# Optimization experiments

Hardware: AMD Instinct MI355X
Metric: run time of the kernel (lower is better)

The kernel has to match this reference:

```python
import jax, jax.numpy as jnp
import numpy as np

NPROTOS = 40      # forced by init_offset_tensor reshape
NCLASS  = 512     # number of child classes
C       = 64      # genetic feature channels (pshape[0])
W       = 40      # genetic sequence width (hard-coded in offset tensor)
B       = 1024    # batch
P       = NPROTOS * NCLASS  # 20480 total prototypes
EPS     = 1e-12   # F.normalize eps


def _build_last_layer_weight():
    # match[j, j // nprotos] = 1, weight = match.T with zeros -> -0.5
    match = np.zeros((P, NCLASS), np.float32)
    match[np.arange(P), np.arange(P) // NPROTOS] = 1.0
    w = match.T.copy()
    w[w == 0] = -0.5
    return jnp.asarray(w)


def _build_offset_tensor():
    # arange2[i, j] = (i - j) % nprotos; nprotos == 40 so arange3 is empty
    i = np.arange(NPROTOS)[:, None]
    j = np.arange(NPROTOS)[None, :]
    ar2 = (i - j) % NPROTOS                                  # (40, 40)
    off = np.tile(ar2.reshape(NPROTOS, 1, 1, NPROTOS), (NCLASS, C, 1, 1))
    return jnp.asarray(off.astype(np.int32))                 # (P, C, 1, W)


def setup_inputs() -> dict:
    key = jax.random.key(0)
    k1, k2 = jax.random.split(key)
    conv_features = jax.random.normal(k1, (B, C, 1, W), dtype=jnp.float32)
    prototype = jax.random.uniform(k2, (P, C, 1, 1), dtype=jnp.float32)  # torch.rand
    return {
        "conv_features": conv_features,
        "prototype": prototype,
        "last_layer_weight": _build_last_layer_weight(),
        "offset_tensor": _build_offset_tensor(),
    }


def _l2norm(x, axis):
    # F.normalize: x / max(||x||_2, eps)
    return x / jnp.maximum(jnp.linalg.norm(x, axis=axis, keepdims=True), EPS)


def reference(conv_features, prototype, last_layer_weight, offset_tensor):
    sqrt_D = 1.0  # sqrt(pshape[1] * pshape[2]) = sqrt(1*1)
    x = _l2norm(conv_features, axis=1) / sqrt_D              # (B, C, 1, W)
    p = _l2norm(prototype, axis=1) / sqrt_D                  # (P, C, 1, 1)
    # pad prototypes to width W, then per-prototype spatial offset gather
    p = jnp.pad(p, ((0, 0), (0, 0), (0, 0), (0, W - 1)))     # (P, C, 1, W)
    p = jnp.take_along_axis(p, offset_tensor, axis=3)        # (P, C, 1, W)
    # conv2d with full-width kernel -> output (B, P, 1, 1); max_pool over 1x1 is identity
    sim = jnp.einsum('bchw,pchw->bp', x, p)                  # (B, P)
    min_distances = -sim                                     # view(-1, nclass*nprotos)
    logits = sim @ last_layer_weight.T                       # (B, NCLASS)
    return (logits, min_distances)
```

## Files before the change

### kernel.cpp

```cpp
#include <hip/hip_runtime.h>
#include <math.h>

#define NB 1024
#define NC 64
#define NW 40
#define NK 512
#define NP 20480
#define EPSF 1e-12f


__global__ __launch_bounds__(256) void knorm_p(const float* __restrict__ proto,
                                               float* __restrict__ pn) {
    int wave = threadIdx.x >> 6;
    int lane = threadIdx.x & 63;
    int p = blockIdx.x * 4 + wave;
    float v = proto[p * 64 + lane];
    float s = v * v;
#pragma unroll
    for (int off = 32; off >= 1; off >>= 1) s += __shfl_xor(s, off);
    float r = 1.0f / fmaxf(sqrtf(s), EPSF);
    int j = p % NW, k = p / NW;
    pn[(j * NK + k) * 64 + lane] = v * r;
}

__global__ __launch_bounds__(256) void knorm_x(const float* __restrict__ x,
                                               float* __restrict__ xn) {
    __shared__ float xs[64 * 41];
    __shared__ float rn[40];
    int b = blockIdx.x;
    const float* xb = x + b * (64 * 40);
    for (int t = threadIdx.x; t < 2560; t += 256) {
        int c = t / 40, w = t % 40;
        xs[c * 41 + w] = xb[t];
    }
    __syncthreads();
    if (threadIdx.x < 40) {
        int w = threadIdx.x;
        float s = 0.f;
#pragma unroll
        for (int c = 0; c < 64; ++c) { float v = xs[c * 41 + w]; s += v * v; }
        rn[w] = 1.0f / fmaxf(sqrtf(s), EPSF);
    }
    __syncthreads();
    for (int t = threadIdx.x; t < 2560; t += 256) {
        int w = t >> 6, c = t & 63;
        xn[(w * NB + b) * 64 + c] = xs[c * 41 + w] * rn[w];
    }
}

__global__ __launch_bounds__(256) void kgemm(const float* __restrict__ xn,
                                             const float* __restrict__ pn,
                                             float* __restrict__ simt) {
    __shared__ float4 Xs[128 * 16];
    __shared__ float4 Ps[128 * 16];
    int b0 = blockIdx.x * 128;
    int k0 = blockIdx.y * 128;
    int j  = blockIdx.z;
    const float4* xg = (const float4*)(xn + (size_t)(j * NB + b0) * 64);
    const float4* pg = (const float4*)(pn + (size_t)(j * NK + k0) * 64);
    for (int g = threadIdx.x; g < 2048; g += 256) {
        int row = g >> 4, c4 = g & 15;
        int idx = (row << 4) + (c4 ^ (row & 15));
        Xs[idx] = xg[g];
        Ps[idx] = pg[g];
    }
    __syncthreads();
    int tb = threadIdx.x >> 4, tk = threadIdx.x & 15;
    float acc[8][8];
#pragma unroll
    for (int i = 0; i < 8; ++i)
#pragma unroll
        for (int q = 0; q < 8; ++q) acc[i][q] = 0.f;

#pragma unroll 2
    for (int c4 = 0; c4 < 16; ++c4) {
        float4 xv[8], pv[8];
#pragma unroll
        for (int i = 0; i < 8; ++i) xv[i] = Xs[((tb + 16 * i) << 4) + (c4 ^ tb)];
#pragma unroll
        for (int q = 0; q < 8; ++q) pv[q] = Ps[((tk + 16 * q) << 4) + (c4 ^ tk)];
#pragma unroll
        for (int i = 0; i < 8; ++i)
#pragma unroll
            for (int q = 0; q < 8; ++q)
                acc[i][q] += xv[i].x * pv[q].x + xv[i].y * pv[q].y +
                             xv[i].z * pv[q].z + xv[i].w * pv[q].w;
    }

#pragma unroll
    for (int i = 0; i < 8; ++i) {
        int b = b0 + tb + 16 * i;
        float* dst = simt + (size_t)b * NP + j * NK + k0;
#pragma unroll
        for (int q = 0; q < 8; ++q) dst[tk + 16 * q] = acc[i][q];
    }
}

__global__ __launch_bounds__(1024) void ktrans(float* __restrict__ out) {
    __shared__ float row[512 * 41];
    __shared__ float red[1024];
    __shared__ float wsum[16];
    __shared__ float tshare;
    int b = blockIdx.x;
    float* md = out + 524288 + (size_t)b * NP;
    int k = threadIdx.x & 511;
    int jh = threadIdx.x >> 9;
    float racc = 0.f;
#pragma unroll 4
    for (int jj = 0; jj < 20; ++jj) {
        int j = jh * 20 + jj;
        float v = md[j * NK + k];
        row[k * 41 + j] = -v;
        racc += v;
    }
    red[threadIdx.x] = racc;
    float t = racc;
#pragma unroll
    for (int off = 32; off >= 1; off >>= 1) t += __shfl_xor(t, off);
    if ((threadIdx.x & 63) == 0) wsum[threadIdx.x >> 6] = t;
    __syncthreads();
    float rk = 0.f;
    if (threadIdx.x < 512) rk = red[threadIdx.x] + red[threadIdx.x + 512];
    if (threadIdx.x == 0) {
        float tt = 0.f;
#pragma unroll
        for (int i = 0; i < 16; ++i) tt += wsum[i];
        tshare = tt;
    }
    __syncthreads();
    if (threadIdx.x < 512)
        out[(size_t)b * NK + threadIdx.x] = 1.5f * rk - 0.5f * tshare;
    for (int t2 = threadIdx.x; t2 < NP; t2 += 1024) {
        int kk = t2 / 40, jj = t2 % 40;
        md[t2] = row[kk * 41 + jj];
    }
}

extern "C" void kernel_launch(void* const* d_in, const int* in_sizes, int n_in,
                              void* d_out, int out_size, void* d_ws, size_t ws_size,
                              hipStream_t stream) {
    (void)in_sizes; (void)n_in; (void)out_size; (void)ws_size;
    const float* conv  = (const float*)d_in[0];
    const float* proto = (const float*)d_in[1];
    float* out = (float*)d_out;
    float* ws = (float*)d_ws;
    float* pn = ws;
    float* xn = ws + 1310720;
    float* simt = out + 524288;

    knorm_p<<<5120, 256, 0, stream>>>(proto, pn);
    knorm_x<<<1024, 256, 0, stream>>>(conv, xn);
    kgemm<<<dim3(8, 4, 40), 256, 0, stream>>>(xn, pn, simt);
    ktrans<<<1024, 1024, 0, stream>>>(out);
}
```

Before: 370.5 us.

## Stage GEMM output in workspace and rework transpose kernel with float4 stores

The GEMM now writes its similarity tile to a separate workspace buffer with contiguous float4 stores, giving each thread eight adjacent prototype columns and a new LDS swizzle. The transpose/logit kernel reads from that buffer rather than transposing in place in the output. It drops from 1024 to 256 threads, processes 128 classes per pass through a small padded LDS tile, and writes the negated distances with float4 stores. This reduces LDS footprint and uncoalesced scalar traffic, at the cost of extra workspace and four barrier-separated passes per block.

```diff
diff --git a/kernel.cpp b/kernel.cpp
--- a/kernel.cpp
+++ b/kernel.cpp
@@ -60,7 +60,7 @@
     const float4* pg = (const float4*)(pn + (size_t)(j * NK + k0) * 64);
     for (int g = threadIdx.x; g < 2048; g += 256) {
         int row = g >> 4, c4 = g & 15;
-        int idx = (row << 4) + (c4 ^ (row & 15));
+        int idx = (row << 4) + (c4 ^ (row >> 3));
         Xs[idx] = xg[g];
         Ps[idx] = pg[g];
     }
@@ -72,67 +72,91 @@
 #pragma unroll
         for (int q = 0; q < 8; ++q) acc[i][q] = 0.f;
 
-#pragma unroll 2
     for (int c4 = 0; c4 < 16; ++c4) {
-        float4 xv[8], pv[8];
+        float4 xv[8];
 #pragma unroll
-        for (int i = 0; i < 8; ++i) xv[i] = Xs[((tb + 16 * i) << 4) + (c4 ^ tb)];
+        for (int i = 0; i < 8; ++i) {
+            int row = tb + 16 * i;
+            xv[i] = Xs[(row << 4) + (c4 ^ (row >> 3))];
+        }
 #pragma unroll
-        for (int q = 0; q < 8; ++q) pv[q] = Ps[((tk + 16 * q) << 4) + (c4 ^ tk)];
+        for (int q = 0; q < 8; ++q) {
+            int row = tk * 8 + q;
+            float4 pv = Ps[(row << 4) + (c4 ^ tk)];
 #pragma unroll
-        for (int i = 0; i < 8; ++i)
-#pragma unroll
-            for (int q = 0; q < 8; ++q)
-                acc[i][q] += xv[i].x * pv[q].x + xv[i].y * pv[q].y +
-                             xv[i].z * pv[q].z + xv[i].w * pv[q].w;
+            for (int i = 0; i < 8; ++i)
+                acc[i][q] += xv[i].x * pv.x + xv[i].y * pv.y +
+                             xv[i].z * pv.z + xv[i].w * pv.w;
+        }
     }
 
 #pragma unroll
     for (int i = 0; i < 8; ++i) {
         int b = b0 + tb + 16 * i;
-        float* dst = simt + (size_t)b * NP + j * NK + k0;
-#pragma unroll
-        for (int q = 0; q < 8; ++q) dst[tk + 16 * q] = acc[i][q];
+        float4* dst = (float4*)(simt + (size_t)b * NP + j * NK + k0 + tk * 8);
+        dst[0] = make_float4(acc[i][0], acc[i][1], acc[i][2], acc[i][3]);
+        dst[1] = make_float4(acc[i][4], acc[i][5], acc[i][6], acc[i][7]);
     }
 }
 
-__global__ __launch_bounds__(1024) void ktrans(float* __restrict__ out) {
-    __shared__ float row[512 * 41];
-    __shared__ float red[1024];
-    __shared__ float wsum[16];
-    __shared__ float tshare;
+__global__ __launch_bounds__(256) void ktrans(const float* __restrict__ simt,
+                                              float* __restrict__ out) {
+    __shared__ float ld[128][41];
+    __shared__ float wred[4];
     int b = blockIdx.x;
-    float* md = out + 524288 + (size_t)b * NP;
-    int k = threadIdx.x & 511;
-    int jh = threadIdx.x >> 9;
-    float racc = 0.f;
-#pragma unroll 4
-    for (int jj = 0; jj < 20; ++jj) {
-        int j = jh * 20 + jj;
-        float v = md[j * NK + k];
-        row[k * 41 + j] = -v;
-        racc += v;
+    int t = threadIdx.x;
+    const float* src = simt + (size_t)b * NP;
+    float* md = out + (size_t)NB * NK + (size_t)b * NP;
+    float rk[4];
+    float my_tot = 0.f;
+
+#pragma unroll
+    for (int pass = 0; pass < 4; ++pass) {
+        int k0 = pass << 7;
+#pragma unroll
+        for (int s = 0; s < 5; ++s) {
+            int idx = s * 256 + t;
+            int jj = idx >> 5, f4 = idx & 31;
+            float4 v = *(const float4*)(src + jj * NK + k0 + f4 * 4);
+            ld[f4 * 4 + 0][jj] = v.x;
+            ld[f4 * 4 + 1][jj] = v.y;
+            ld[f4 * 4 + 2][jj] = v.z;
+            ld[f4 * 4 + 3][jj] = v.w;
+        }
+        __syncthreads();
+        if (t < 128) {
+            float s = 0.f;
+#pragma unroll
+            for (int jj = 0; jj < 40; ++jj) s += ld[t][jj];
+            rk[pass] = s;
+            my_tot += s;
+        }
+#pragma unroll
+        for (int s2 = 0; s2 < 5; ++s2) {
+            int pl = s2 * 1024 + t * 4;
+            int kk = pl / 40;
+            int jj = pl - kk * 40;
+            float vv[4];
+#pragma unroll
+            for (int e = 0; e < 4; ++e) {
+                vv[e] = -ld[kk][jj];
+                if (++jj == 40) { jj = 0; ++kk; }
+            }
+            *(float4*)(md + k0 * 40 + pl) = make_float4(vv[0], vv[1], vv[2], vv[3]);
+        }
+        __syncthreads();
     }
-    red[threadIdx.x] = racc;
-    float t = racc;
+
+    float s = my_tot;
 #pragma unroll
-    for (int off = 32; off >= 1; off >>= 1) t += __shfl_xor(t, off);
-    if ((threadIdx.x & 63) == 0) wsum[threadIdx.x >> 6] = t;
+    for (int off = 32; off >= 1; off >>= 1) s += __shfl_xor(s, off);
+    if ((t & 63) == 0) wred[t >> 6] = s;
     __syncthreads();
-    float rk = 0.f;
-    if (threadIdx.x < 512) rk = red[threadIdx.x] + red[threadIdx.x + 512];
-    if (threadIdx.x == 0) {
-        float tt = 0.f;
+    float S = wred[0] + wred[1] + wred[2] + wred[3];
+    if (t < 128) {
 #pragma unroll
-        for (int i = 0; i < 16; ++i) tt += wsum[i];
-        tshare = tt;
-    }
-    __syncthreads();
-    if (threadIdx.x < 512)
-        out[(size_t)b * NK + threadIdx.x] = 1.5f * rk - 0.5f * tshare;
-    for (int t2 = threadIdx.x; t2 < NP; t2 += 1024) {
-        int kk = t2 / 40, jj = t2 % 40;
-        md[t2] = row[kk * 41 + jj];
+        for (int pass = 0; pass < 4; ++pass)
+            out[(size_t)b * NK + (pass << 7) + t] = 1.5f * rk[pass] - 0.5f * S;
     }
 }
 
@@ -144,12 +168,12 @@
     const float* proto = (const float*)d_in[1];
     float* out = (float*)d_out;
     float* ws = (float*)d_ws;
-    float* pn = ws;
-    float* xn = ws + 1310720;
-    float* simt = out + 524288;
+    float* pn   = ws;
+    float* xn   = ws + 1310720;
+    float* simt = ws + 3932160;
 
     knorm_p<<<5120, 256, 0, stream>>>(proto, pn);
     knorm_x<<<1024, 256, 0, stream>>>(conv, xn);
     kgemm<<<dim3(8, 4, 40), 256, 0, stream>>>(xn, pn, simt);
-    ktrans<<<1024, 1024, 0, stream>>>(out);
+    ktrans<<<1024, 256, 0, stream>>>(simt, out);
 }
```

New measurement: 355.8 us. -4.0%, faster.
